# Performance work log

Hardware: AMD Instinct MI355X
Metric: run time of the kernel (lower is better)

The kernel has to match this reference:

```python
import jax, jax.numpy as jnp
import numpy as np

NUM_HEADS = 8
MASK_RATE = 0.5


def setup_inputs() -> dict:
    key = jax.random.key(0)
    ks = jax.random.split(key, 6)
    B, N, C = 8, 1024, 256
    TABLE = 10
    att_embedding = jax.random.normal(ks[0], (B, N, C), dtype=jnp.float32)
    relation_position = jax.random.randint(ks[1], (B, N, N), 0, TABLE, dtype=jnp.int32)
    rel_len = jax.random.randint(ks[2], (B,), 0, 20, dtype=jnp.int32)
    W_qkv = jax.random.normal(ks[3], (C, 3 * C), dtype=jnp.float32) * (1.0 / np.sqrt(C))
    W_proj = jax.random.normal(ks[4], (C, C), dtype=jnp.float32) * (1.0 / np.sqrt(C))
    b_proj = jnp.zeros((C,), dtype=jnp.float32)
    bias_table = jax.random.normal(ks[5], (TABLE, NUM_HEADS), dtype=jnp.float32) * 0.02
    return {
        "att_embedding": att_embedding,
        "relation_position": relation_position,
        "rel_len": rel_len,
        "W_qkv": W_qkv,
        "W_proj": W_proj,
        "b_proj": b_proj,
        "bias_table": bias_table,
    }


def reference(att_embedding, relation_position, rel_len, W_qkv, W_proj, b_proj, bias_table):
    B, N, C = att_embedding.shape
    H = NUM_HEADS
    hd = C // H
    scale = hd ** -0.5

    # QKV projection (no bias): [B,N,3C] -> q,k,v each [B,H,N,hd]
    qkv = (att_embedding @ W_qkv).reshape(B, N, 3, H, hd)
    qkv = jnp.transpose(qkv, (2, 0, 3, 1, 4))
    q, k, v = qkv[0], qkv[1], qkv[2]

    # Attention scores [B,H,N,N]
    attn = jnp.einsum("bhnd,bhmd->bhnm", q, k) * scale

    # Relative position bias: gather [B,N,N,H] -> [B,H,N,N]
    pos_bias = jnp.transpose(bias_table[relation_position], (0, 3, 1, 2))

    # Mask bias: table row t gets -100 iff t > mask_len (mask_len+1 .. TABLE-1);
    # identical across heads -> compute as [B,1,N,N] instead of materializing [B,H,N,N].
    mask_len = (rel_len.astype(jnp.float32) * MASK_RATE).astype(jnp.int32)
    mask_bias = jnp.where(relation_position > mask_len[:, None, None], -100.0, 0.0)[:, None]

    attn = jax.nn.softmax(attn + pos_bias + mask_bias, axis=-1)

    # Weighted values -> [B,N,C] -> output projection
    x = jnp.einsum("bhnm,bhmd->bnhd", attn, v).reshape(B, N, C)
    x = x @ W_proj + b_proj
    return x
```

## Files before the change

kernel.cpp:

```cpp
#include <hip/hip_runtime.h>
#include <hip/hip_bf16.h>

typedef __bf16 bf16;
typedef __bf16 bf16x2 __attribute__((ext_vector_type(2)));
typedef __bf16 bf16x8 __attribute__((ext_vector_type(8)));
typedef float f32x4 __attribute__((ext_vector_type(4)));
typedef int i32x4 __attribute__((ext_vector_type(4)));

#define B_ 8
#define N_ 1024
#define C_ 256
#define H_ 8
#define C3_ 768
#define SCALE 0.17677669529663689f
#define FMAX 16.0f


__global__ __launch_bounds__(256) void prep(
    const float* __restrict__ Wqkv, const float* __restrict__ Wproj,
    const int* __restrict__ rel,
    bf16* __restrict__ Wq_tiled, bf16* __restrict__ Wp_tiled,
    unsigned char* __restrict__ rel8)
{
  int bb = blockIdx.x;
  if (bb < 768) {
    int o = bb * 256 + threadIdx.x;
    int kk = o & 31;
    int idx = o >> 5;
    int nr = idx & 63;
    int qq = idx >> 6;
    int nt = qq % 12, kt = qq / 12;
    int n = nt * 64 + nr, k = kt * 32 + kk;
    Wq_tiled[o] = (bf16)Wqkv[k * C3_ + n];
  } else if (bb < 1024) {
    int p = (bb - 768) * 256 + threadIdx.x;
    int kk = p & 31;
    int n = (p >> 5) & 255;
    int kt = p >> 13;
    int k = kt * 32 + kk;
    Wp_tiled[p] = (bf16)Wproj[k * C_ + n];
  } else {
    long p = ((long)(bb - 1024) * 256 + threadIdx.x) * 16;
    i32x4 a = *reinterpret_cast<const i32x4*>(rel + p);
    i32x4 b2 = *reinterpret_cast<const i32x4*>(rel + p + 4);
    i32x4 c = *reinterpret_cast<const i32x4*>(rel + p + 8);
    i32x4 d = *reinterpret_cast<const i32x4*>(rel + p + 12);
    unsigned o0 = (unsigned)a[0] | ((unsigned)a[1] << 8) | ((unsigned)a[2] << 16) | ((unsigned)a[3] << 24);
    unsigned o1 = (unsigned)b2[0] | ((unsigned)b2[1] << 8) | ((unsigned)b2[2] << 16) | ((unsigned)b2[3] << 24);
    unsigned o2 = (unsigned)c[0] | ((unsigned)c[1] << 8) | ((unsigned)c[2] << 16) | ((unsigned)c[3] << 24);
    unsigned o3 = (unsigned)d[0] | ((unsigned)d[1] << 8) | ((unsigned)d[2] << 16) | ((unsigned)d[3] << 24);
    i32x4 ov = {(int)o0, (int)o1, (int)o2, (int)o3};
    *reinterpret_cast<i32x4*>(rel8 + p) = ov;
  }
}

__global__ __launch_bounds__(256) void gemm_qkv(
    const float* __restrict__ A, const bf16* __restrict__ Wq_tiled,
    bf16* __restrict__ q, bf16* __restrict__ kT, bf16* __restrict__ vT)
{
  __shared__ bf16 As[128][40];
  __shared__ bf16 Bts[128][40];
  __shared__ bf16 Vls[64][136];

  int tid = threadIdx.x;
  int wave = tid >> 6, lane = tid & 63, quad = lane >> 4, l16 = lane & 15;
  int m0 = blockIdx.x * 128, n0 = blockIdx.y * 128;
  int msub = (wave & 1) * 64, nsub = (wave >> 1) * 64;

  f32x4 acc[4][4] = {};

  int arow = tid >> 1, akc = (tid & 1) * 16;
  const float* aptr = A + (long)(m0 + arow) * C_ + akc;
  int bn = tid >> 1, bkc = (tid & 1) * 16;
  const bf16* bptr = Wq_tiled +
      ((long)(blockIdx.y * 2 + (bn >> 6)) * 2048 + (bn & 63) * 32 + bkc);

  float4 a0 = *reinterpret_cast<const float4*>(aptr);
  float4 a1 = *reinterpret_cast<const float4*>(aptr + 4);
  float4 a2 = *reinterpret_cast<const float4*>(aptr + 8);
  float4 a3 = *reinterpret_cast<const float4*>(aptr + 12);
  i32x4 bv0 = *reinterpret_cast<const i32x4*>(bptr);
  i32x4 bv1 = *reinterpret_cast<const i32x4*>(bptr + 8);

  for (int kt = 0; kt < 8; ++kt) {
    __syncthreads();
    {
      bf16 at[16] = {(bf16)a0.x, (bf16)a0.y, (bf16)a0.z, (bf16)a0.w,
                     (bf16)a1.x, (bf16)a1.y, (bf16)a1.z, (bf16)a1.w,
                     (bf16)a2.x, (bf16)a2.y, (bf16)a2.z, (bf16)a2.w,
                     (bf16)a3.x, (bf16)a3.y, (bf16)a3.z, (bf16)a3.w};
      *reinterpret_cast<bf16x8*>(&As[arow][akc]) = *reinterpret_cast<bf16x8*>(at);
      *reinterpret_cast<bf16x8*>(&As[arow][akc + 8]) = *reinterpret_cast<bf16x8*>(at + 8);
      *reinterpret_cast<i32x4*>(&Bts[bn][bkc]) = bv0;
      *reinterpret_cast<i32x4*>(&Bts[bn][bkc + 8]) = bv1;
    }
    __syncthreads();

    if (kt < 7) {
      int kn = (kt + 1) * 32;
      a0 = *reinterpret_cast<const float4*>(aptr + kn);
      a1 = *reinterpret_cast<const float4*>(aptr + kn + 4);
      a2 = *reinterpret_cast<const float4*>(aptr + kn + 8);
      a3 = *reinterpret_cast<const float4*>(aptr + kn + 12);
      bv0 = *reinterpret_cast<const i32x4*>(bptr + (long)(kt + 1) * 24576);
      bv1 = *reinterpret_cast<const i32x4*>(bptr + (long)(kt + 1) * 24576 + 8);
    }

    bf16x8 af[4], bfr[4];
#pragma unroll
    for (int mi = 0; mi < 4; ++mi)
      af[mi] = *reinterpret_cast<const bf16x8*>(&As[msub + mi * 16 + l16][quad * 8]);
#pragma unroll
    for (int ni = 0; ni < 4; ++ni)
      bfr[ni] = *reinterpret_cast<const bf16x8*>(&Bts[nsub + ni * 16 + l16][quad * 8]);
#pragma unroll
    for (int mi = 0; mi < 4; ++mi)
#pragma unroll
      for (int ni = 0; ni < 4; ++ni)
        acc[mi][ni] = __builtin_amdgcn_mfma_f32_16x16x32_bf16(af[mi], bfr[ni], acc[mi][ni], 0, 0, 0);
  }

  if (n0 < 256) {
#pragma unroll
    for (int mi = 0; mi < 4; ++mi)
#pragma unroll
      for (int ni = 0; ni < 4; ++ni)
#pragma unroll
        for (int r = 0; r < 4; ++r) {
          int row = m0 + msub + mi * 16 + quad * 4 + r;
          int col = n0 + nsub + ni * 16 + l16;
          q[(long)row * 256 + col] = (bf16)(acc[mi][ni][r] * SCALE);
        }
  } else if (n0 < 512) {
#pragma unroll
    for (int mi = 0; mi < 4; ++mi)
#pragma unroll
      for (int ni = 0; ni < 4; ++ni)
#pragma unroll
        for (int r = 0; r < 4; ++r) {
          int row = m0 + msub + mi * 16 + quad * 4 + r;
          int c = n0 + nsub + ni * 16 + l16 - 256;
          int b = row >> 10, n = row & 1023;
          int h = c >> 5, d = c & 31;
          kT[(((long)(b * H_ + h)) * N_ + n) * 32 + d] = (bf16)acc[mi][ni][r];
        }
  } else {
    int b = m0 >> 10;
#pragma unroll
    for (int ch = 0; ch < 2; ++ch) {
      __syncthreads();
      if ((nsub >> 6) == ch) {
#pragma unroll
        for (int mi = 0; mi < 4; ++mi)
#pragma unroll
          for (int ni = 0; ni < 4; ++ni)
#pragma unroll
            for (int r = 0; r < 4; ++r) {
              int cc = ni * 16 + l16;
              int nn = msub + mi * 16 + quad * 4 + r;
              int np = (nn & 96) | ((nn & 12) << 1) | (nn & 3) | (((nn >> 4) & 1) << 2);
              Vls[cc][np] = (bf16)acc[mi][ni][r];
            }
      }
      __syncthreads();
      int cc = tid >> 2, nseg = (tid & 3) * 32;
      long base = ((long)(b * C_ + (n0 - 512) + ch * 64 + cc)) * N_ + (m0 & 1023) + nseg;
#pragma unroll
      for (int j = 0; j < 4; ++j)
        *reinterpret_cast<i32x4*>(vT + base + j * 8) =
            *reinterpret_cast<const i32x4*>(&Vls[cc][nseg + j * 8]);
    }
  }
}

__global__ __launch_bounds__(512) void flash_attn(
    const bf16* __restrict__ q, const bf16* __restrict__ kT,
    const bf16* __restrict__ vT, const unsigned char* __restrict__ rel8,
    const int* __restrict__ rel_len, const float* __restrict__ btab,
    const bf16* __restrict__ Wp_tiled, const float* __restrict__ bias,
    float* __restrict__ out)
{
  __shared__ __align__(16) char smem[78336];
  char* const KB0 = smem;
  char* const VB0 = smem + 32768;
  char* const RB0 = smem + 65536;
  float* const ebtl = (float*)(smem + 77824);

  int tid = threadIdx.x;
  int h = tid >> 6, lane = tid & 63, quad = lane >> 4, l16 = lane & 15;

  int wg = blockIdx.y * 64 + blockIdx.x;
  int swz = (wg & 7) * 64 + (wg >> 3);
  int b = swz >> 6, i0 = (swz & 63) * 16;
  long bN = (long)b * N_;

  int mask_len = (int)((float)rel_len[b] * 0.5f);
  if (tid < 80) {
    int t = tid >> 3, hh = tid & 7;
    ebtl[hh * 16 + t] = __expf(btab[t * H_ + hh] + (t > mask_len ? -100.f : 0.f) - FMAX);
  }

  bf16x8 qf = *reinterpret_cast<const bf16x8*>(
      q + (bN + i0 + l16) * 256 + h * 32 + quad * 8);

  __syncthreads();

  int l = lane;
  int sxc = (((l & 3) ^ ((l >> 3) & 3)) << 4);
  int kc0 = (l >> 2) * 64 + sxc;
  int vc0 = (h * 32 + (l >> 2)) * 2048 + sxc;
  int rc0 = (l >> 3) * 1024 + (l & 7) * 4;

  const char* kTb = (const char*)kT + ((long)(b * 8 + h) << 16);
  const char* vTb = (const char*)vT + (long)b * 524288;
  const char* rb8 = (const char*)rel8 + (bN + i0) * 1024;

  int swq = ((quad ^ ((l16 >> 1) & 3)) << 4);
  int kr = h * 2048 + l16 * 64 + swq;
  int rr = h * 512 + l16 * 32 + quad * 4;

#define KB(i) (KB0 + (i) * 16384)
#define VB(i) (VB0 + (i) * 16384)
#define RB(i) (RB0 + (i) * 4096)

#define GLD16(G, L) __builtin_amdgcn_global_load_lds(                         \
    (const __attribute__((address_space(1))) void*)(G),                       \
    (__attribute__((address_space(3))) void*)(L), 16, 0, 0)
#define GLD4(G, L) __builtin_amdgcn_global_load_lds(                          \
    (const __attribute__((address_space(1))) void*)(G),                       \
    (__attribute__((address_space(3))) void*)(L), 4, 0, 0)

#define GATH(G, RV0, RV1) do {                                                \
    _Pragma("unroll")                                                         \
    for (int e = 0; e < 4; ++e) {                                             \
      G[e]     = ebtl[h * 16 + (int)((RV0 >> (8 * e)) & 255u)];               \
      G[4 + e] = ebtl[h * 16 + (int)((RV1 >> (8 * e)) & 255u)];               \
    }                                                                         \
  } while (0)

#define COMP(K0, K1, V0, V1, G) do {                                          \
    f32x4 z = {};                                                             \
    f32x4 s0 = __builtin_amdgcn_mfma_f32_16x16x32_bf16(K0, qf, z, 0, 0, 0);   \
    f32x4 s1 = __builtin_amdgcn_mfma_f32_16x16x32_bf16(K1, qf, z, 0, 0, 0);   \
    bf16x8 pa;                                                                \
    _Pragma("unroll")                                                         \
    for (int e = 0; e < 4; ++e) {                                             \
      float p0 = __expf(s0[e]) * G[e];                                        \
      float p1 = __expf(s1[e]) * G[4 + e];                                    \
      l_acc += p0 + p1;                                                       \
      pa[e] = (bf16)p0;                                                       \
      pa[4 + e] = (bf16)p1;                                                   \
    }                                                                         \
    oacc[0] = __builtin_amdgcn_mfma_f32_16x16x32_bf16(pa, V0, oacc[0], 0, 0, 0); \
    oacc[1] = __builtin_amdgcn_mfma_f32_16x16x32_bf16(pa, V1, oacc[1], 0, 0, 0); \
  } while (0)

#define TILE(T_, KVR, KVW, RR_, RW_, GC, GN) do {                             \
    int tn_ = ((T_) + 1) & 31, tr_ = ((T_) + 3) & 31;                         \
    GLD16(kTb + tn_ * 2048 + kc0,        KB(KVW) + h * 2048);                 \
    GLD16(kTb + tn_ * 2048 + kc0 + 1024, KB(KVW) + h * 2048 + 1024);          \
    GLD16(vTb + tn_ * 64 + vc0,          VB(KVW) + h * 2048);                 \
    GLD16(vTb + tn_ * 64 + vc0 + 32768,  VB(KVW) + h * 2048 + 1024);          \
    GLD4(rb8 + tr_ * 32 + rc0,           RB(RW_) + h * 512);                  \
    GLD4(rb8 + tr_ * 32 + rc0 + 8192,    RB(RW_) + h * 512 + 256);            \
    asm volatile("s_waitcnt vmcnt(8)" ::: "memory");                          \
    bf16x8 kf0 = *(const bf16x8*)(KB(KVR) + kr);                              \
    bf16x8 kf1 = *(const bf16x8*)(KB(KVR) + kr + 1024);                       \
    bf16x8 vf0 = *(const bf16x8*)(VB(KVR) + kr);                              \
    bf16x8 vf1 = *(const bf16x8*)(VB(KVR) + kr + 1024);                       \
    unsigned rv0 = *(const unsigned*)(RB(RR_) + rr);                          \
    unsigned rv1 = *(const unsigned*)(RB(RR_) + rr + 16);                     \
    GATH(GN, rv0, rv1);                                                       \
    COMP(kf0, kf1, vf0, vf1, GC);                                             \
  } while (0)

  f32x4 oacc[2] = {};
  float l_acc = 0.f;
  float gA[8], gB[8];

  GLD16(kTb + kc0,        KB(0) + h * 2048);
  GLD16(kTb + kc0 + 1024, KB(0) + h * 2048 + 1024);
  GLD16(vTb + vc0,          VB(0) + h * 2048);
  GLD16(vTb + vc0 + 32768,  VB(0) + h * 2048 + 1024);
  GLD4(rb8 + rc0,             RB(0) + h * 512);
  GLD4(rb8 + rc0 + 8192,      RB(0) + h * 512 + 256);
  GLD4(rb8 + 32 + rc0,        RB(1) + h * 512);
  GLD4(rb8 + 32 + rc0 + 8192, RB(1) + h * 512 + 256);
  GLD4(rb8 + 64 + rc0,        RB(2) + h * 512);
  GLD4(rb8 + 64 + rc0 + 8192, RB(2) + h * 512 + 256);
  asm volatile("s_waitcnt vmcnt(2)" ::: "memory");
  {
    unsigned rv0 = *(const unsigned*)(RB(0) + rr);
    unsigned rv1 = *(const unsigned*)(RB(0) + rr + 16);
    GATH(gA, rv0, rv1);
  }

#pragma unroll 1
  for (int t = 0; t < 30; t += 6) {
    TILE(t + 0, 0, 1, 1, 0, gA, gB);
    TILE(t + 1, 1, 0, 2, 1, gB, gA);
    TILE(t + 2, 0, 1, 0, 2, gA, gB);
    TILE(t + 3, 1, 0, 1, 0, gB, gA);
    TILE(t + 4, 0, 1, 2, 1, gA, gB);
    TILE(t + 5, 1, 0, 0, 2, gB, gA);
  }
  TILE(30, 0, 1, 1, 0, gA, gB);
  TILE(31, 1, 0, 2, 1, gB, gA);
#undef TILE
#undef COMP
#undef GATH
#undef GLD16
#undef GLD4
#undef KB
#undef VB
#undef RB

  asm volatile("s_waitcnt vmcnt(0)" ::: "memory");
  __syncthreads();

  float lsum = l_acc;
  lsum += __shfl_xor(lsum, 16);
  lsum += __shfl_xor(lsum, 32);
  float inv = 1.f / lsum;

  bf16 (*attL)[264] = (bf16(*)[264])(void*)smem;
#pragma unroll
  for (int r = 0; r < 4; ++r) {
    float invr = __shfl(inv, quad * 4 + r);
    attL[quad * 4 + r][h * 32 + l16] = (bf16)(oacc[0][r] * invr);
    attL[quad * 4 + r][h * 32 + 16 + l16] = (bf16)(oacc[1][r] * invr);
  }
  __syncthreads();

  f32x4 pacc[2] = {};
  const bf16* wp = Wp_tiled + ((h * 32 + l16) * 32 + quad * 8);
#pragma unroll
  for (int kt = 0; kt < 8; ++kt) {
    bf16x8 afr = *reinterpret_cast<const bf16x8*>(&attL[l16][kt * 32 + quad * 8]);
    bf16x8 b0 = *reinterpret_cast<const bf16x8*>(wp + kt * 8192);
    bf16x8 b1 = *reinterpret_cast<const bf16x8*>(wp + kt * 8192 + 512);
    pacc[0] = __builtin_amdgcn_mfma_f32_16x16x32_bf16(afr, b0, pacc[0], 0, 0, 0);
    pacc[1] = __builtin_amdgcn_mfma_f32_16x16x32_bf16(afr, b1, pacc[1], 0, 0, 0);
  }
  float bi0 = bias[h * 32 + l16];
  float bi1 = bias[h * 32 + 16 + l16];
#pragma unroll
  for (int r = 0; r < 4; ++r) {
    long rowoff = (bN + i0 + quad * 4 + r) * C_ + h * 32;
    out[rowoff + l16] = pacc[0][r] + bi0;
    out[rowoff + 16 + l16] = pacc[1][r] + bi1;
  }
}

extern "C" void kernel_launch(void* const* d_in, const int* in_sizes, int n_in,
                              void* d_out, int out_size, void* d_ws, size_t ws_size,
                              hipStream_t stream) {
  const float* X     = (const float*)d_in[0];
  const int*   rel   = (const int*)d_in[1];
  const int*   rlen  = (const int*)d_in[2];
  const float* Wqkv  = (const float*)d_in[3];
  const float* Wproj = (const float*)d_in[4];
  const float* bproj = (const float*)d_in[5];
  const float* btab  = (const float*)d_in[6];
  float* out = (float*)d_out;

  char* ws = (char*)d_ws;
  bf16* Wq_tiled = (bf16*)ws;
  bf16* Wp_tiled = (bf16*)(ws + 393216);
  bf16* q  = (bf16*)(ws + 524288);
  bf16* kT = (bf16*)(ws + 524288 + 4194304);
  bf16* vT = (bf16*)(ws + 524288 + 2 * 4194304);
  unsigned char* rel8 = (unsigned char*)(ws + 13107200);

  prep<<<dim3(3072), 256, 0, stream>>>(Wqkv, Wproj, rel, Wq_tiled, Wp_tiled, rel8);
  gemm_qkv<<<dim3(8192 / 128, C3_ / 128), 256, 0, stream>>>(X, Wq_tiled, q, kT, vT);
  flash_attn<<<dim3(N_ / 16, B_), 512, 0, stream>>>(
      q, kT, vT, rel8, rlen, btab, Wp_tiled, bproj, out);
}
```

Before: 140.6 us.

## Move rel8/Wproj prep into QKV GEMM grid, halve M tile, stage epilogue via LDS

The rel-position int32→uint8 packing and the Wproj tiling move out of the prep kernel and into extra blocks of the QKV GEMM launch, so they run alongside the GEMM instead of before it. The GEMM M tile shrinks from 128 to 64 rows, giving more blocks for better CU fill. Q and K outputs are now staged through shared memory so they leave as 16-byte coalesced stores instead of scalar bf16 writes. The flash kernel's initial wait changes from vmcnt(2) to vmcnt(0), which may add a small stall; the smaller tile also lowers operand reuse per block.

```diff
diff --git a/kernel.cpp b/kernel.cpp
--- a/kernel.cpp
+++ b/kernel.cpp
@@ -17,82 +17,81 @@
 
 
 __global__ __launch_bounds__(256) void prep(
-    const float* __restrict__ Wqkv, const float* __restrict__ Wproj,
-    const int* __restrict__ rel,
-    bf16* __restrict__ Wq_tiled, bf16* __restrict__ Wp_tiled,
-    unsigned char* __restrict__ rel8)
+    const float* __restrict__ Wqkv, bf16* __restrict__ Wq_tiled)
 {
-  int bb = blockIdx.x;
-  if (bb < 768) {
-    int o = bb * 256 + threadIdx.x;
-    int kk = o & 31;
-    int idx = o >> 5;
-    int nr = idx & 63;
-    int qq = idx >> 6;
-    int nt = qq % 12, kt = qq / 12;
-    int n = nt * 64 + nr, k = kt * 32 + kk;
-    Wq_tiled[o] = (bf16)Wqkv[k * C3_ + n];
-  } else if (bb < 1024) {
-    int p = (bb - 768) * 256 + threadIdx.x;
-    int kk = p & 31;
-    int n = (p >> 5) & 255;
-    int kt = p >> 13;
-    int k = kt * 32 + kk;
-    Wp_tiled[p] = (bf16)Wproj[k * C_ + n];
-  } else {
-    long p = ((long)(bb - 1024) * 256 + threadIdx.x) * 16;
-    i32x4 a = *reinterpret_cast<const i32x4*>(rel + p);
-    i32x4 b2 = *reinterpret_cast<const i32x4*>(rel + p + 4);
-    i32x4 c = *reinterpret_cast<const i32x4*>(rel + p + 8);
-    i32x4 d = *reinterpret_cast<const i32x4*>(rel + p + 12);
-    unsigned o0 = (unsigned)a[0] | ((unsigned)a[1] << 8) | ((unsigned)a[2] << 16) | ((unsigned)a[3] << 24);
-    unsigned o1 = (unsigned)b2[0] | ((unsigned)b2[1] << 8) | ((unsigned)b2[2] << 16) | ((unsigned)b2[3] << 24);
-    unsigned o2 = (unsigned)c[0] | ((unsigned)c[1] << 8) | ((unsigned)c[2] << 16) | ((unsigned)c[3] << 24);
-    unsigned o3 = (unsigned)d[0] | ((unsigned)d[1] << 8) | ((unsigned)d[2] << 16) | ((unsigned)d[3] << 24);
-    i32x4 ov = {(int)o0, (int)o1, (int)o2, (int)o3};
-    *reinterpret_cast<i32x4*>(rel8 + p) = ov;
-  }
+  int o = blockIdx.x * 256 + threadIdx.x;
+  int kk = o & 31;
+  int idx = o >> 5;
+  int nr = idx & 63;
+  int qq = idx >> 6;
+  int nt = qq % 12, kt = qq / 12;
+  int n = nt * 64 + nr, k = kt * 32 + kk;
+  Wq_tiled[o] = (bf16)Wqkv[k * C3_ + n];
 }
 
 __global__ __launch_bounds__(256) void gemm_qkv(
     const float* __restrict__ A, const bf16* __restrict__ Wq_tiled,
-    bf16* __restrict__ q, bf16* __restrict__ kT, bf16* __restrict__ vT)
+    const float* __restrict__ Wproj, const int* __restrict__ rel,
+    bf16* __restrict__ q, bf16* __restrict__ kT, bf16* __restrict__ vT,
+    bf16* __restrict__ Wp_tiled, unsigned char* __restrict__ rel8)
 {
-  __shared__ bf16 As[128][40];
-  __shared__ bf16 Bts[128][40];
-  __shared__ bf16 Vls[64][136];
-
+  __shared__ __align__(16) char sm[18432];
+
+  int bb = blockIdx.x;
   int tid = threadIdx.x;
+
+  if (bb >= 768) {
+    if (bb < 2816) {
+      long p = ((long)(bb - 768) * 256 + tid) * 16;
+      i32x4 a = *reinterpret_cast<const i32x4*>(rel + p);
+      i32x4 b2 = *reinterpret_cast<const i32x4*>(rel + p + 4);
+      i32x4 c = *reinterpret_cast<const i32x4*>(rel + p + 8);
+      i32x4 d = *reinterpret_cast<const i32x4*>(rel + p + 12);
+      unsigned o0 = (unsigned)a[0] | ((unsigned)a[1] << 8) | ((unsigned)a[2] << 16) | ((unsigned)a[3] << 24);
+      unsigned o1 = (unsigned)b2[0] | ((unsigned)b2[1] << 8) | ((unsigned)b2[2] << 16) | ((unsigned)b2[3] << 24);
+      unsigned o2 = (unsigned)c[0] | ((unsigned)c[1] << 8) | ((unsigned)c[2] << 16) | ((unsigned)c[3] << 24);
+      unsigned o3 = (unsigned)d[0] | ((unsigned)d[1] << 8) | ((unsigned)d[2] << 16) | ((unsigned)d[3] << 24);
+      i32x4 ov = {(int)o0, (int)o1, (int)o2, (int)o3};
+      *reinterpret_cast<i32x4*>(rel8 + p) = ov;
+    } else {
+      int p = (bb - 2816) * 256 + tid;
+      int kk = p & 31;
+      int n = (p >> 5) & 255;
+      int kt = p >> 13;
+      Wp_tiled[p] = (bf16)Wproj[(kt * 32 + kk) * C_ + n];
+    }
+    return;
+  }
+
+  bf16 (*As)[40] = (bf16(*)[40])(void*)sm;
+  bf16 (*Bs)[40] = (bf16(*)[40])(void*)(sm + 5120);
+
   int wave = tid >> 6, lane = tid & 63, quad = lane >> 4, l16 = lane & 15;
-  int m0 = blockIdx.x * 128, n0 = blockIdx.y * 128;
-  int msub = (wave & 1) * 64, nsub = (wave >> 1) * 64;
-
-  f32x4 acc[4][4] = {};
-
-  int arow = tid >> 1, akc = (tid & 1) * 16;
+  int x = bb & 127, y = bb >> 7;
+  int m0 = x * 64, n0 = y * 128;
+  int msub = (wave & 1) * 32, nsub = (wave >> 1) * 64;
+
+  f32x4 acc[2][4] = {};
+
+  int arow = tid >> 2, akc = (tid & 3) * 8;
   const float* aptr = A + (long)(m0 + arow) * C_ + akc;
   int bn = tid >> 1, bkc = (tid & 1) * 16;
   const bf16* bptr = Wq_tiled +
-      ((long)(blockIdx.y * 2 + (bn >> 6)) * 2048 + (bn & 63) * 32 + bkc);
+      ((long)(y * 2 + (bn >> 6)) * 2048 + (bn & 63) * 32 + bkc);
 
   float4 a0 = *reinterpret_cast<const float4*>(aptr);
   float4 a1 = *reinterpret_cast<const float4*>(aptr + 4);
-  float4 a2 = *reinterpret_cast<const float4*>(aptr + 8);
-  float4 a3 = *reinterpret_cast<const float4*>(aptr + 12);
   i32x4 bv0 = *reinterpret_cast<const i32x4*>(bptr);
   i32x4 bv1 = *reinterpret_cast<const i32x4*>(bptr + 8);
 
   for (int kt = 0; kt < 8; ++kt) {
     __syncthreads();
     {
-      bf16 at[16] = {(bf16)a0.x, (bf16)a0.y, (bf16)a0.z, (bf16)a0.w,
-                     (bf16)a1.x, (bf16)a1.y, (bf16)a1.z, (bf16)a1.w,
-                     (bf16)a2.x, (bf16)a2.y, (bf16)a2.z, (bf16)a2.w,
-                     (bf16)a3.x, (bf16)a3.y, (bf16)a3.z, (bf16)a3.w};
+      bf16 at[8] = {(bf16)a0.x, (bf16)a0.y, (bf16)a0.z, (bf16)a0.w,
+                    (bf16)a1.x, (bf16)a1.y, (bf16)a1.z, (bf16)a1.w};
       *reinterpret_cast<bf16x8*>(&As[arow][akc]) = *reinterpret_cast<bf16x8*>(at);
-      *reinterpret_cast<bf16x8*>(&As[arow][akc + 8]) = *reinterpret_cast<bf16x8*>(at + 8);
-      *reinterpret_cast<i32x4*>(&Bts[bn][bkc]) = bv0;
-      *reinterpret_cast<i32x4*>(&Bts[bn][bkc + 8]) = bv1;
+      *reinterpret_cast<i32x4*>(&Bs[bn][bkc]) = bv0;
+      *reinterpret_cast<i32x4*>(&Bs[bn][bkc + 8]) = bv1;
     }
     __syncthreads();
 
@@ -100,76 +99,80 @@
       int kn = (kt + 1) * 32;
       a0 = *reinterpret_cast<const float4*>(aptr + kn);
       a1 = *reinterpret_cast<const float4*>(aptr + kn + 4);
-      a2 = *reinterpret_cast<const float4*>(aptr + kn + 8);
-      a3 = *reinterpret_cast<const float4*>(aptr + kn + 12);
       bv0 = *reinterpret_cast<const i32x4*>(bptr + (long)(kt + 1) * 24576);
       bv1 = *reinterpret_cast<const i32x4*>(bptr + (long)(kt + 1) * 24576 + 8);
     }
 
-    bf16x8 af[4], bfr[4];
-#pragma unroll
-    for (int mi = 0; mi < 4; ++mi)
+    bf16x8 af[2], bfr[4];
+#pragma unroll
+    for (int mi = 0; mi < 2; ++mi)
       af[mi] = *reinterpret_cast<const bf16x8*>(&As[msub + mi * 16 + l16][quad * 8]);
 #pragma unroll
     for (int ni = 0; ni < 4; ++ni)
-      bfr[ni] = *reinterpret_cast<const bf16x8*>(&Bts[nsub + ni * 16 + l16][quad * 8]);
-#pragma unroll
-    for (int mi = 0; mi < 4; ++mi)
+      bfr[ni] = *reinterpret_cast<const bf16x8*>(&Bs[nsub + ni * 16 + l16][quad * 8]);
+#pragma unroll
+    for (int mi = 0; mi < 2; ++mi)
 #pragma unroll
       for (int ni = 0; ni < 4; ++ni)
         acc[mi][ni] = __builtin_amdgcn_mfma_f32_16x16x32_bf16(af[mi], bfr[ni], acc[mi][ni], 0, 0, 0);
   }
 
-  if (n0 < 256) {
-#pragma unroll
-    for (int mi = 0; mi < 4; ++mi)
+  __syncthreads();
+
+  if (y < 4) {
+    float mul = (y < 2) ? SCALE : 1.0f;
+    bf16 (*Ep)[136] = (bf16(*)[136])(void*)sm;
+#pragma unroll
+    for (int mi = 0; mi < 2; ++mi)
 #pragma unroll
       for (int ni = 0; ni < 4; ++ni)
 #pragma unroll
+        for (int r = 0; r < 4; ++r)
+          Ep[msub + mi * 16 + quad * 4 + r][nsub + ni * 16 + l16] =
+              (bf16)(acc[mi][ni][r] * mul);
+    __syncthreads();
+    int row = tid >> 2, seg = tid & 3;
+    i32x4 w0 = *reinterpret_cast<const i32x4*>(&Ep[row][seg * 32]);
+    i32x4 w1 = *reinterpret_cast<const i32x4*>(&Ep[row][seg * 32 + 8]);
+    i32x4 w2 = *reinterpret_cast<const i32x4*>(&Ep[row][seg * 32 + 16]);
+    i32x4 w3 = *reinterpret_cast<const i32x4*>(&Ep[row][seg * 32 + 24]);
+    bf16* dst;
+    if (y < 2) {
+      dst = q + (long)(m0 + row) * 256 + n0 + seg * 32;
+    } else {
+      int c = n0 - 256 + seg * 32;
+      int h = c >> 5;
+      int gr = m0 + row, b = gr >> 10, n = gr & 1023;
+      dst = kT + (((long)(b * H_ + h)) * N_ + n) * 32;
+    }
+    *reinterpret_cast<i32x4*>(dst) = w0;
+    *reinterpret_cast<i32x4*>(dst + 8) = w1;
+    *reinterpret_cast<i32x4*>(dst + 16) = w2;
+    *reinterpret_cast<i32x4*>(dst + 24) = w3;
+  } else {
+    bf16 (*Vls)[72] = (bf16(*)[72])(void*)sm;
+#pragma unroll
+    for (int mi = 0; mi < 2; ++mi)
+#pragma unroll
+      for (int ni = 0; ni < 4; ++ni)
+#pragma unroll
         for (int r = 0; r < 4; ++r) {
-          int row = m0 + msub + mi * 16 + quad * 4 + r;
-          int col = n0 + nsub + ni * 16 + l16;
-          q[(long)row * 256 + col] = (bf16)(acc[mi][ni][r] * SCALE);
+          int nn = msub + mi * 16 + quad * 4 + r;
+          int np = (nn & ~31) | ((nn & 12) << 1) | (nn & 3) | (((nn >> 4) & 1) << 2);
+          Vls[nsub + ni * 16 + l16][np] = (bf16)acc[mi][ni][r];
         }
-  } else if (n0 < 512) {
-#pragma unroll
-    for (int mi = 0; mi < 4; ++mi)
-#pragma unroll
-      for (int ni = 0; ni < 4; ++ni)
-#pragma unroll
-        for (int r = 0; r < 4; ++r) {
-          int row = m0 + msub + mi * 16 + quad * 4 + r;
-          int c = n0 + nsub + ni * 16 + l16 - 256;
-          int b = row >> 10, n = row & 1023;
-          int h = c >> 5, d = c & 31;
-          kT[(((long)(b * H_ + h)) * N_ + n) * 32 + d] = (bf16)acc[mi][ni][r];
-        }
-  } else {
-    int b = m0 >> 10;
-#pragma unroll
-    for (int ch = 0; ch < 2; ++ch) {
-      __syncthreads();
-      if ((nsub >> 6) == ch) {
-#pragma unroll
-        for (int mi = 0; mi < 4; ++mi)
-#pragma unroll
-          for (int ni = 0; ni < 4; ++ni)
-#pragma unroll
-            for (int r = 0; r < 4; ++r) {
-              int cc = ni * 16 + l16;
-              int nn = msub + mi * 16 + quad * 4 + r;
-              int np = (nn & 96) | ((nn & 12) << 1) | (nn & 3) | (((nn >> 4) & 1) << 2);
-              Vls[cc][np] = (bf16)acc[mi][ni][r];
-            }
-      }
-      __syncthreads();
-      int cc = tid >> 2, nseg = (tid & 3) * 32;
-      long base = ((long)(b * C_ + (n0 - 512) + ch * 64 + cc)) * N_ + (m0 & 1023) + nseg;
-#pragma unroll
-      for (int j = 0; j < 4; ++j)
-        *reinterpret_cast<i32x4*>(vT + base + j * 8) =
-            *reinterpret_cast<const i32x4*>(&Vls[cc][nseg + j * 8]);
-    }
+    __syncthreads();
+    int c = tid >> 1, nseg = (tid & 1) * 32;
+    i32x4 w0 = *reinterpret_cast<const i32x4*>(&Vls[c][nseg]);
+    i32x4 w1 = *reinterpret_cast<const i32x4*>(&Vls[c][nseg + 8]);
+    i32x4 w2 = *reinterpret_cast<const i32x4*>(&Vls[c][nseg + 16]);
+    i32x4 w3 = *reinterpret_cast<const i32x4*>(&Vls[c][nseg + 24]);
+    int gb = m0 >> 10, mn = m0 & 1023;
+    bf16* dst = vT + ((long)(gb * C_ + n0 - 512 + c)) * N_ + mn + nseg;
+    *reinterpret_cast<i32x4*>(dst) = w0;
+    *reinterpret_cast<i32x4*>(dst + 8) = w1;
+    *reinterpret_cast<i32x4*>(dst + 16) = w2;
+    *reinterpret_cast<i32x4*>(dst + 24) = w3;
   }
 }
 
@@ -288,7 +291,7 @@
   GLD4(rb8 + 32 + rc0 + 8192, RB(1) + h * 512 + 256);
   GLD4(rb8 + 64 + rc0,        RB(2) + h * 512);
   GLD4(rb8 + 64 + rc0 + 8192, RB(2) + h * 512 + 256);
-  asm volatile("s_waitcnt vmcnt(2)" ::: "memory");
+  asm volatile("s_waitcnt vmcnt(0)" ::: "memory");
   {
     unsigned rv0 = *(const unsigned*)(RB(0) + rr);
     unsigned rv1 = *(const unsigned*)(RB(0) + rr + 16);
@@ -372,8 +375,9 @@
   bf16* vT = (bf16*)(ws + 524288 + 2 * 4194304);
   unsigned char* rel8 = (unsigned char*)(ws + 13107200);
 
-  prep<<<dim3(3072), 256, 0, stream>>>(Wqkv, Wproj, rel, Wq_tiled, Wp_tiled, rel8);
-  gemm_qkv<<<dim3(8192 / 128, C3_ / 128), 256, 0, stream>>>(X, Wq_tiled, q, kT, vT);
+  prep<<<dim3(768), 256, 0, stream>>>(Wqkv, Wq_tiled);
+  gemm_qkv<<<dim3(3072), 256, 0, stream>>>(X, Wq_tiled, Wproj, rel,
+                                           q, kT, vT, Wp_tiled, rel8);
   flash_attn<<<dim3(N_ / 16, B_), 512, 0, stream>>>(
       q, kT, vT, rel8, rlen, btab, Wp_tiled, bproj, out);
 }
```

After: 138.8 us. Within noise of the previous version (-1.3%).
